# Kernel optimization log

Measured on AMD Instinct MI355X. Metric: run time of the kernel, lower is better.

Reference implementation:

```python
import jax, jax.numpy as jnp
import numpy as np

EMBED_DIM = 512
Q_DIM = 64
V_DIM = 64
WINDOW_SIZE = 128
B, N = 2, 4096


def setup_inputs() -> dict:
    key = jax.random.key(0)
    ks = jax.random.split(key, 7)
    s = 1.0 / np.sqrt(EMBED_DIM)
    u = lambda k, shape: jax.random.uniform(k, shape, jnp.float32, -s, s)
    return {
        "x": jax.random.normal(ks[0], (B, N, EMBED_DIM), jnp.float32),
        "Wq": u(ks[1], (EMBED_DIM, Q_DIM)),
        "bq": u(ks[2], (Q_DIM,)),
        "Wk": u(ks[3], (EMBED_DIM, Q_DIM)),
        "bk": u(ks[4], (Q_DIM,)),
        "Wv": u(ks[5], (EMBED_DIM, V_DIM)),
        "bv": u(ks[6], (V_DIM,)),
    }


def reference(x, Wq, bq, Wk, bk, Wv, bv):
    b, n, _ = x.shape
    w = WINDOW_SIZE // 2
    Q = x @ Wq + bq  # (b, n, Qd)
    K = x @ Wk + bk  # (b, n, Qd)
    V = x @ Wv + bv  # (b, n, Vd)

    diags = jnp.arange(-w, w + 1)            # (nd,) offsets di
    nd = diags.shape[0]
    # Gather K[i + di] via padded K; invalid positions masked to 0 afterwards.
    Kpad = jnp.pad(K, ((0, 0), (w, w), (0, 0)))
    j = jnp.arange(n)[:, None] + diags[None, :]          # (n, nd) = i + di
    Kg = Kpad[:, j + w, :]                               # (b, n, nd, Qd)
    scores = jnp.einsum('bnd,bnod->bno', Q, Kg)          # (b, n, nd)
    valid = (j >= 0) & (j < n)
    scores = jnp.where(valid[None], scores, 0.0)

    # Faithful to original: diagonal dot products are scattered into the FIRST
    # nd columns of a dense (b, n, n) matrix (rest zeros), softmax over the
    # full n columns, then dense matmul with V.
    columns = jnp.zeros((b, n, n), dtype=x.dtype).at[:, :, :nd].set(scores)
    attn = jax.nn.softmax(columns, axis=2)               # (b, n, n)
    return attn @ V                                      # (b, n, Vd)
```

## Files before the change

### kernel.cpp

```cpp
#include <hip/hip_runtime.h>

typedef _Float16 half8 __attribute__((ext_vector_type(8)));
typedef float f32x4 __attribute__((ext_vector_type(4)));

#define NN 4096
#define NE 512
#define HD 64
#define KROWS 4288
#define KOFF  64
#define WSCALE (1.0f / 256.0f)

__device__ __forceinline__ void f16_split(float f, _Float16& hi, _Float16& lo) {
    hi = (_Float16)f;
    lo = (_Float16)(f - (float)hi);
}

#define MFMA16(a, b, c) __builtin_amdgcn_mfma_f32_16x16x32_f16((a), (b), (c), 0, 0, 0)

__global__ __launch_bounds__(256) void wprep_kernel(
    const float* __restrict__ Wq, const float* __restrict__ Wk,
    const float* __restrict__ Wv,
    _Float16* __restrict__ Wf, _Float16* __restrict__ Khi,
    _Float16* __restrict__ Vf, float* __restrict__ Vs)
{
    const int gtid = blockIdx.x * 256 + threadIdx.x;
    const int L = gtid & 63;
    {
        const int nt = (gtid >> 6) % 12;
        const int kt = gtid / 768;
        const int n = nt * 16 + (L & 15);
        const int kbase = kt * 32 + (L >> 4) * 8;
        const float* src; int col;
        if (n < 64)       { src = Wq; col = n; }
        else if (n < 128) { src = Wk; col = n - 64; }
        else              { src = Wv; col = n - 128; }
        half8 sh;
#pragma unroll
        for (int j = 0; j < 8; ++j)
            sh[j] = (_Float16)src[(size_t)(kbase + j) * HD + col];
        *(half8*)(Wf + (size_t)gtid * 8) = sh;
    }
    if (gtid < 6144) {
        const int p = gtid >> 3, o = gtid & 7;
        const int b = p / 192, q = p - b * 192;
        const size_t row = (size_t)b * KROWS + (q < 64 ? q : 4096 + q);
        const half8 z = {0, 0, 0, 0, 0, 0, 0, 0};
        *(half8*)(Khi + row * HD + o * 8) = z;
    }
    if (gtid < 3200) {
        const int rem = gtid % 1600;
        const int jt = rem / 320;
        const int nt = (rem / 64) % 5;
        half8 sh = {0, 0, 0, 0, 0, 0, 0, 0};
        if (nt == 4 && (L & 15) == 0) {
#pragma unroll
            for (int jj = 0; jj < 8; ++jj) {
                const int j = jt * 32 + (L >> 4) * 8 + jj;
                if (j < 129) sh[jj] = (_Float16)1.0f;
            }
        }
        *(half8*)(Vf + (size_t)gtid * 8) = sh;
    }
    if (gtid < 128) Vs[gtid] = 0.f;
}

__global__ __launch_bounds__(512) void proj_kernel(
    const float* __restrict__ x, const _Float16* __restrict__ Wf,
    const float* __restrict__ bq, const float* __restrict__ bk,
    const float* __restrict__ bv,
    _Float16* __restrict__ Qhi, _Float16* __restrict__ Qlo,
    _Float16* __restrict__ Khi, _Float16* __restrict__ Vf,
    float* __restrict__ Vs)
{
    __shared__ float parts[4][3][64][4];
    __shared__ float V_lds[16][68];
    const int tid = threadIdx.x;
    const int L = tid & 63;
    const int w = tid >> 6;
    const int m = L & 15, kg = L >> 4;
    const int blk = blockIdx.x;
    const int r0 = blk * 16;
    const int b = blk >> 8;
    const int t3 = w & 3;
    const int h = w >> 2;

    const float* xp = x + (size_t)(r0 + m) * NE + h * 256 + kg * 8;
    const _Float16* wfb = Wf + ((size_t)(h * 8) * 12 + t3 * 3) * 512 + L * 8;

    f32x4 acc[3];
#pragma unroll
    for (int t = 0; t < 3; ++t) acc[t] = (f32x4){0.f, 0.f, 0.f, 0.f};

#pragma unroll
    for (int kt = 0; kt < 8; ++kt) {
        const float4 x0 = *(const float4*)(xp + kt * 32);
        const float4 x1 = *(const float4*)(xp + kt * 32 + 4);
        const float xv[8] = {x0.x, x0.y, x0.z, x0.w, x1.x, x1.y, x1.z, x1.w};
        half8 ahi, alo;
#pragma unroll
        for (int j = 0; j < 8; ++j) {
            _Float16 hh, ll; f16_split(xv[j], hh, ll);
            ahi[j] = hh; alo[j] = ll;
        }
#pragma unroll
        for (int t = 0; t < 3; ++t) {
            const half8 wv = *(const half8*)(wfb + (size_t)kt * 6144 + t * 512);
            acc[t] = MFMA16(ahi, wv, acc[t]);
            acc[t] = MFMA16(alo, wv, acc[t]);
        }
    }

    if (h == 1) {
#pragma unroll
        for (int t = 0; t < 3; ++t)
            *(f32x4*)(&parts[t3][t][L][0]) = acc[t];
    }
    __syncthreads();

    if (h == 0) {
#pragma unroll
        for (int t = 0; t < 3; ++t) {
            const f32x4 p = *(const f32x4*)(&parts[t3][t][L][0]);
            acc[t] += p;
            const int nt = t3 * 3 + t;
            const int cgc = nt * 16 + m;
            const float bias = (cgc < 64) ? bq[cgc]
                             : (cgc < 128) ? bk[cgc - 64] : bv[cgc - 128];
#pragma unroll
            for (int r = 0; r < 4; ++r) {
                const int gr = r0 + kg * 4 + r;
                const float val = acc[t][r] + bias;
                if (cgc < 64) {
                    _Float16 hh, ll; f16_split(val, hh, ll);
                    Qhi[(size_t)gr * HD + cgc] = hh;
                    Qlo[(size_t)gr * HD + cgc] = ll;
                } else if (cgc < 128) {
                    const int d = cgc - 64, n = gr & 4095;
                    Khi[((size_t)b * KROWS + KOFF + n) * HD + d] = (_Float16)val;
                } else {
                    V_lds[kg * 4 + r][cgc - 128] = val;
                }
            }
        }
    }
    __syncthreads();

    if (tid < 64) {
        float s = 0.f;
#pragma unroll
        for (int r = 0; r < 16; ++r) s += V_lds[r][tid];
        atomicAdd(&Vs[b * HD + tid], s);
    }

    {
        const int local = blk & 255;
        if (local < 8 && w < 4) {
            const int jt = local >> 1;
            if ((kg >> 1) == (local & 1)) {
                const int nt = w;
                half8 sh;
#pragma unroll
                for (int jj = 0; jj < 8; ++jj) {
                    const int lrow = (kg - (local & 1) * 2) * 8 + jj;
                    sh[jj] = (_Float16)V_lds[lrow][nt * 16 + m];
                }
                const size_t fo = ((size_t)((b * 25 + jt * 5 + nt) * 64 + L)) * 8;
                *(half8*)(Vf + fo) = sh;
            }
        } else if (local == 8 && w < 4 && kg == 0) {
            const int nt = w;
            half8 sh = {0, 0, 0, 0, 0, 0, 0, 0};
            sh[0] = (_Float16)V_lds[0][nt * 16 + m];
            const size_t fo = ((size_t)((b * 25 + 4 * 5 + nt) * 64 + L)) * 8;
            *(half8*)(Vf + fo) = sh;
        }
    }
}

__global__ __launch_bounds__(256) void attn_kernel(
    const _Float16* __restrict__ Qhi, const _Float16* __restrict__ Qlo,
    const _Float16* __restrict__ Khi, const _Float16* __restrict__ Vf,
    const float* __restrict__ Vs, float* __restrict__ out)
{
    __shared__ __align__(16) _Float16 wt_hi[16 * 168];
    __shared__ __align__(16) _Float16 wt_lo[16 * 168];
    __shared__ float den_lds[16];

    const int tid = threadIdx.x;
    const int L = tid & 63;
    const int w = tid >> 6;
    const int m = L & 15, kg = L >> 4;
    const int b = blockIdx.x >> 8;
    const int n0 = (blockIdx.x & 255) * 16;

    const _Float16* qp  = Qhi + ((size_t)(b * NN + n0 + m)) * HD + kg * 8;
    const _Float16* qp2 = Qlo + ((size_t)(b * NN + n0 + m)) * HD + kg * 8;
    const half8 qhi0 = *(const half8*)(qp);
    const half8 qhi1 = *(const half8*)(qp + 32);
    const half8 qlo0 = *(const half8*)(qp2);
    const half8 qlo1 = *(const half8*)(qp2 + 32);

    int kts[3]; int nkt;
    if (w == 3) { kts[0] = 3; kts[1] = 7; kts[2] = 8; nkt = 3; }
    else        { kts[0] = w; kts[1] = w + 4; kts[2] = 0; nkt = 2; }

    const _Float16* KB = Khi + (size_t)b * KROWS * HD;
    half8 kh0[3], kh1[3];
#pragma unroll
    for (int i = 0; i < 3; ++i) {
        if (i < nkt) {
            const _Float16* kp = KB + (size_t)(n0 + kts[i] * 16 + m) * HD + kg * 8;
            kh0[i] = *(const half8*)(kp);
            kh1[i] = *(const half8*)(kp + 32);
        }
    }

    half8 vhi[5], vh4[5];
#pragma unroll
    for (int jt = 0; jt < 5; ++jt) {
        const size_t fo = ((size_t)((b * 25 + jt * 5 + w) * 64 + L)) * 8;
        vhi[jt] = *(const half8*)(Vf + fo);
    }
    if (w == 0) {
#pragma unroll
        for (int jt = 0; jt < 5; ++jt) {
            const size_t fo4 = ((size_t)((b * 25 + jt * 5 + 4) * 64 + L)) * 8;
            vh4[jt] = *(const half8*)(Vf + fo4);
        }
    }

    for (int i = tid; i < (16 * 168) / 2; i += 256) {
        ((int*)wt_hi)[i] = 0;
        ((int*)wt_lo)[i] = 0;
    }
    __syncthreads();

#pragma unroll
    for (int i = 0; i < 3; ++i) {
        if (i < nkt) {
            f32x4 acc = (f32x4){0.f, 0.f, 0.f, 0.f};
            acc = MFMA16(qhi0, kh0[i], acc);
            acc = MFMA16(qhi1, kh1[i], acc);
            acc = MFMA16(qlo0, kh0[i], acc);
            acc = MFMA16(qlo1, kh1[i], acc);
            const int l = kts[i] * 16 + m;
#pragma unroll
            for (int r = 0; r < 4; ++r) {
                const int q = kg * 4 + r;
                const int j = l - q;
                if (j >= 0 && j < 129) {
                    const float wval = (__expf(acc[r]) - 1.0f) * WSCALE;
                    _Float16 hh, ll; f16_split(wval, hh, ll);
                    wt_hi[q * 168 + j] = hh;
                    wt_lo[q * 168 + j] = ll;
                }
            }
        }
    }
    __syncthreads();

    f32x4 oacc = (f32x4){0.f, 0.f, 0.f, 0.f};
    f32x4 dacc = (f32x4){0.f, 0.f, 0.f, 0.f};
#pragma unroll
    for (int jt = 0; jt < 5; ++jt) {
        const half8 whi = *(const half8*)(wt_hi + m * 168 + jt * 32 + kg * 8);
        const half8 wlo = *(const half8*)(wt_lo + m * 168 + jt * 32 + kg * 8);
        oacc = MFMA16(whi, vhi[jt], oacc);
        oacc = MFMA16(wlo, vhi[jt], oacc);
        if (w == 0) {
            dacc = MFMA16(whi, vh4[jt], dacc);
            dacc = MFMA16(wlo, vh4[jt], dacc);
        }
    }
    if (w == 0 && m == 0) {
#pragma unroll
        for (int r = 0; r < 4; ++r) den_lds[kg * 4 + r] = dacc[r];
    }
    __syncthreads();

    {
        const float vs = Vs[b * HD + w * 16 + m];
#pragma unroll
        for (int r = 0; r < 4; ++r) {
            const int q = kg * 4 + r;
            const float val = (vs + 256.0f * oacc[r])
                            / (4096.f + 256.0f * den_lds[q]);
            out[((size_t)(b * NN + n0 + q)) * HD + w * 16 + m] = val;
        }
    }
}

extern "C" void kernel_launch(void* const* d_in, const int* in_sizes, int n_in,
                              void* d_out, int out_size, void* d_ws, size_t ws_size,
                              hipStream_t stream)
{
    const float* x  = (const float*)d_in[0];
    const float* Wq = (const float*)d_in[1];
    const float* bq = (const float*)d_in[2];
    const float* Wk = (const float*)d_in[3];
    const float* bk = (const float*)d_in[4];
    const float* Wv = (const float*)d_in[5];
    const float* bv = (const float*)d_in[6];
    float* out = (float*)d_out;

    char* ws = (char*)d_ws;
    float*     Vs  = (float*)(ws + 0);
    _Float16*  Khi = (_Float16*)(ws + 512);
    _Float16*  Qhi = (_Float16*)(ws + 1098240);
    _Float16*  Qlo = (_Float16*)(ws + 2146816);
    _Float16*  Wf  = (_Float16*)(ws + 3195392);
    _Float16*  Vf  = (_Float16*)(ws + 3392000);

    wprep_kernel<<<48, 256, 0, stream>>>(Wq, Wk, Wv, Wf, Khi, Vf, Vs);
    proj_kernel<<<512, 512, 0, stream>>>(x, Wf, bq, bk, bv,
                                         Qhi, Qlo, Khi, Vf, Vs);
    attn_kernel<<<512, 256, 0, stream>>>(Qhi, Qlo, Khi, Vf, Vs, out);
}
```

Measured before the change: 97.89 us.

## Double proj rows per block, trim attn LDS zeroing to tail, hoist Vs load

The projection kernel now handles 32 rows per block with 1024 threads (256 blocks), so the V-feature writes and Vs atomics are issued half as often and the per-block work is larger. The warp-to-tile mapping is reshuffled and the split-K reduction is kept per row-tile. The attention kernel zeroes only the unused tail columns of the weight LDS tiles and drops a barrier. It also loads Vs early to hide its latency. The larger blocks may lower occupancy and raise register pressure.

```diff
diff --git a/kernel.cpp b/kernel.cpp
--- a/kernel.cpp
+++ b/kernel.cpp
@@ -64,7 +64,7 @@
     if (gtid < 128) Vs[gtid] = 0.f;
 }
 
-__global__ __launch_bounds__(512) void proj_kernel(
+__global__ __launch_bounds__(1024, 4) void proj_kernel(
     const float* __restrict__ x, const _Float16* __restrict__ Wf,
     const float* __restrict__ bq, const float* __restrict__ bk,
     const float* __restrict__ bv,
@@ -72,19 +72,21 @@
     _Float16* __restrict__ Khi, _Float16* __restrict__ Vf,
     float* __restrict__ Vs)
 {
-    __shared__ float parts[4][3][64][4];
-    __shared__ float V_lds[16][68];
+    __shared__ float parts[2][4][3][64][4];
+    __shared__ float V_lds[32][68];
     const int tid = threadIdx.x;
     const int L = tid & 63;
     const int w = tid >> 6;
     const int m = L & 15, kg = L >> 4;
     const int blk = blockIdx.x;
-    const int r0 = blk * 16;
-    const int b = blk >> 8;
-    const int t3 = w & 3;
-    const int h = w >> 2;
-
-    const float* xp = x + (size_t)(r0 + m) * NE + h * 256 + kg * 8;
+    const int b = blk >> 7;
+    const int mt = w >> 3;
+    const int t3 = (w >> 1) & 3;
+    const int h = w & 1;
+    const int r0 = blk * 32;
+    const int rr = r0 + mt * 16;
+
+    const float* xp = x + (size_t)(rr + m) * NE + h * 256 + kg * 8;
     const _Float16* wfb = Wf + ((size_t)(h * 8) * 12 + t3 * 3) * 512 + L * 8;
 
     f32x4 acc[3];
@@ -113,14 +115,14 @@
     if (h == 1) {
 #pragma unroll
         for (int t = 0; t < 3; ++t)
-            *(f32x4*)(&parts[t3][t][L][0]) = acc[t];
+            *(f32x4*)(&parts[mt][t3][t][L][0]) = acc[t];
     }
     __syncthreads();
 
     if (h == 0) {
 #pragma unroll
         for (int t = 0; t < 3; ++t) {
-            const f32x4 p = *(const f32x4*)(&parts[t3][t][L][0]);
+            const f32x4 p = *(const f32x4*)(&parts[mt][t3][t][L][0]);
             acc[t] += p;
             const int nt = t3 * 3 + t;
             const int cgc = nt * 16 + m;
@@ -128,7 +130,7 @@
                              : (cgc < 128) ? bk[cgc - 64] : bv[cgc - 128];
 #pragma unroll
             for (int r = 0; r < 4; ++r) {
-                const int gr = r0 + kg * 4 + r;
+                const int gr = rr + kg * 4 + r;
                 const float val = acc[t][r] + bias;
                 if (cgc < 64) {
                     _Float16 hh, ll; f16_split(val, hh, ll);
@@ -138,7 +140,7 @@
                     const int d = cgc - 64, n = gr & 4095;
                     Khi[((size_t)b * KROWS + KOFF + n) * HD + d] = (_Float16)val;
                 } else {
-                    V_lds[kg * 4 + r][cgc - 128] = val;
+                    V_lds[mt * 16 + kg * 4 + r][cgc - 128] = val;
                 }
             }
         }
@@ -148,26 +150,22 @@
     if (tid < 64) {
         float s = 0.f;
 #pragma unroll
-        for (int r = 0; r < 16; ++r) s += V_lds[r][tid];
+        for (int r = 0; r < 32; ++r) s += V_lds[r][tid];
         atomicAdd(&Vs[b * HD + tid], s);
     }
 
     {
-        const int local = blk & 255;
-        if (local < 8 && w < 4) {
-            const int jt = local >> 1;
-            if ((kg >> 1) == (local & 1)) {
-                const int nt = w;
-                half8 sh;
-#pragma unroll
-                for (int jj = 0; jj < 8; ++jj) {
-                    const int lrow = (kg - (local & 1) * 2) * 8 + jj;
-                    sh[jj] = (_Float16)V_lds[lrow][nt * 16 + m];
-                }
-                const size_t fo = ((size_t)((b * 25 + jt * 5 + nt) * 64 + L)) * 8;
-                *(half8*)(Vf + fo) = sh;
-            }
-        } else if (local == 8 && w < 4 && kg == 0) {
+        const int local = blk & 127;
+        if (local < 4 && w < 4) {
+            const int jt = local;
+            const int nt = w;
+            half8 sh;
+#pragma unroll
+            for (int jj = 0; jj < 8; ++jj)
+                sh[jj] = (_Float16)V_lds[kg * 8 + jj][nt * 16 + m];
+            const size_t fo = ((size_t)((b * 25 + jt * 5 + nt) * 64 + L)) * 8;
+            *(half8*)(Vf + fo) = sh;
+        } else if (local == 4 && w < 4 && kg == 0) {
             const int nt = w;
             half8 sh = {0, 0, 0, 0, 0, 0, 0, 0};
             sh[0] = (_Float16)V_lds[0][nt * 16 + m];
@@ -193,6 +191,8 @@
     const int b = blockIdx.x >> 8;
     const int n0 = (blockIdx.x & 255) * 16;
 
+    const float vs = Vs[b * HD + w * 16 + m];
+
     const _Float16* qp  = Qhi + ((size_t)(b * NN + n0 + m)) * HD + kg * 8;
     const _Float16* qp2 = Qlo + ((size_t)(b * NN + n0 + m)) * HD + kg * 8;
     const half8 qhi0 = *(const half8*)(qp);
@@ -229,11 +229,13 @@
         }
     }
 
-    for (int i = tid; i < (16 * 168) / 2; i += 256) {
-        ((int*)wt_hi)[i] = 0;
-        ((int*)wt_lo)[i] = 0;
-    }
-    __syncthreads();
+    for (int t = tid; t < 1248; t += 256) {
+        const int bufsel = t >= 624;
+        const int idx = bufsel ? t - 624 : t;
+        const int q = idx / 39;
+        const int j = 129 + (idx - q * 39);
+        (bufsel ? wt_lo : wt_hi)[q * 168 + j] = (_Float16)0.f;
+    }
 
 #pragma unroll
     for (int i = 0; i < 3; ++i) {
@@ -279,7 +281,6 @@
     __syncthreads();
 
     {
-        const float vs = Vs[b * HD + w * 16 + m];
 #pragma unroll
         for (int r = 0; r < 4; ++r) {
             const int q = kg * 4 + r;
@@ -312,7 +313,7 @@
     _Float16*  Vf  = (_Float16*)(ws + 3392000);
 
     wprep_kernel<<<48, 256, 0, stream>>>(Wq, Wk, Wv, Wf, Khi, Vf, Vs);
-    proj_kernel<<<512, 512, 0, stream>>>(x, Wf, bq, bk, bv,
-                                         Qhi, Qlo, Khi, Vf, Vs);
+    proj_kernel<<<256, 1024, 0, stream>>>(x, Wf, bq, bk, bv,
+                                          Qhi, Qlo, Khi, Vf, Vs);
     attn_kernel<<<512, 256, 0, stream>>>(Qhi, Qlo, Khi, Vf, Vs, out);
 }
```

New measurement: 95.63 us. 1.02x faster.
